# Optimization experiments

Measured on AMD Instinct MI355X. Metric: run time of the kernel, lower is better.

The kernel has to match this reference:

```python
import jax, jax.numpy as jnp
import numpy as np

N = 100000
E = 3200000
EPS = 1e-5


def setup_inputs() -> dict:
    key = jax.random.key(0)
    ks = jax.random.split(key, 12)
    inp = {
        "x": jax.random.normal(ks[0], (N, 512), dtype=jnp.float32),
        "rows": jax.random.randint(ks[1], (E,), 0, N, dtype=jnp.int32),
        "cols": jax.random.randint(ks[2], (E,), 0, N, dtype=jnp.int32),
        "adj_vals": jax.random.uniform(ks[3], (E,), dtype=jnp.float32),
        "w0": jax.random.normal(ks[4], (512, 256), dtype=jnp.float32) * (1.0 / np.sqrt(512)),
        "b0": jnp.zeros((256,), dtype=jnp.float32),
        "w1": jax.random.normal(ks[5], (256, 128), dtype=jnp.float32) * (1.0 / np.sqrt(256)),
        "b1": jnp.zeros((128,), dtype=jnp.float32),
        "dw0": jax.random.normal(ks[6], (128, 256), dtype=jnp.float32) * (1.0 / np.sqrt(128)),
        "db0": jnp.zeros((256,), dtype=jnp.float32),
        "dw1": jax.random.normal(ks[7], (256, 512), dtype=jnp.float32) * (1.0 / np.sqrt(256)),
        "db1": jnp.zeros((512,), dtype=jnp.float32),
    }
    return inp


def _spmm(rows, cols, vals, h):
    # sparse adj (COO) @ dense h : gather neighbor rows, scale, scatter-add
    return jax.ops.segment_sum(vals[:, None] * h[cols], rows, num_segments=N)


def _bn(h):
    # BatchNorm1d(affine=False, track_running_stats=False): batch stats, biased var
    m = h.mean(axis=0)
    v = h.var(axis=0)
    return (h - m) / jnp.sqrt(v + EPS)


def reference(x, rows, cols, adj_vals, w0, b0, w1, b1, dw0, db0, dw1, db1):
    # encoder: 512 -> 256 (relu, bn) -> 128
    h = _spmm(rows, cols, adj_vals, x @ w0) + b0
    h = _bn(jax.nn.relu(h))
    x_out = _spmm(rows, cols, adj_vals, h @ w1) + b1
    # decoder: relu -> 128 -> 256 (relu, bn) -> 512
    r = jax.nn.relu(x_out)
    r = _spmm(rows, cols, adj_vals, r @ dw0) + db0
    r = _bn(jax.nn.relu(r))
    x_rec = _spmm(rows, cols, adj_vals, r @ dw1) + db1
    return (x_out, x_rec)
```

## Files before the change

kernel.cpp:

```cpp
#include <hip/hip_runtime.h>


typedef _Float16 half2v __attribute__((ext_vector_type(2)));
typedef _Float16 half4v __attribute__((ext_vector_type(4)));
typedef _Float16 half8v __attribute__((ext_vector_type(8)));
typedef float f32x4 __attribute__((ext_vector_type(4)));

__global__ void cast_f32_to_f16(const float* __restrict__ in, _Float16* __restrict__ out,
                                size_t n4) {
    const size_t i = (size_t)blockIdx.x * blockDim.x + threadIdx.x;
    if (i >= n4) return;
    const float4 v = ((const float4*)in)[i];
    half4v h;
    h.x = (_Float16)v.x; h.y = (_Float16)v.y; h.z = (_Float16)v.z; h.w = (_Float16)v.w;
    ((half4v*)out)[i] = h;
}

__global__ void cast_transpose_w(const float* __restrict__ W, _Float16* __restrict__ Wt,
                                 int Kin, int Kout) {
    const int idx = blockIdx.x * blockDim.x + threadIdx.x;
    if (idx >= Kin * Kout) return;
    const int c = idx / Kin;
    const int k = idx - c * Kin;
    Wt[idx] = (_Float16)W[(size_t)k * Kout + c];
}

template <bool OUT_F16, bool HAS_BIAS>
__global__ __launch_bounds__(256) void gemm_f16(const _Float16* __restrict__ A,
                                                const _Float16* __restrict__ Wt,
                                                const float* __restrict__ bias,
                                                void* __restrict__ C,
                                                int Nrows, int Kin, int Kout) {
    __shared__ __align__(16) _Float16 As[128][40];
    __shared__ __align__(16) _Float16 Bs[128][40];
    const int tid = threadIdx.x;
    const int r0 = blockIdx.y * 128;
    const int c0 = blockIdx.x * 128;
    const int w = tid >> 6;
    const int lane = tid & 63;
    const int wm = (w >> 1) << 6;
    const int wn = (w & 1) << 6;
    const int lrow = lane & 15;
    const int lk = (lane >> 4) << 3;

    f32x4 acc[4][4];
#pragma unroll
    for (int i = 0; i < 4; ++i)
#pragma unroll
        for (int j = 0; j < 4; ++j) acc[i][j] = f32x4{0.f, 0.f, 0.f, 0.f};

    for (int k0 = 0; k0 < Kin; k0 += 32) {
#pragma unroll
        for (int q = 0; q < 2; ++q) {
            const int c = tid + (q << 8);
            const int row = c >> 2;
            const int kc = (c & 3) << 3;
            half8v av = half8v{0, 0, 0, 0, 0, 0, 0, 0};
            const int gr = r0 + row;
            if (gr < Nrows) av = *(const half8v*)(A + (size_t)gr * Kin + (k0 + kc));
            *(half8v*)&As[row][kc] = av;
            const half8v wv = *(const half8v*)(Wt + (size_t)(c0 + row) * Kin + (k0 + kc));
            *(half8v*)&Bs[row][kc] = wv;
        }
        __syncthreads();

        half8v af[4], bf[4];
#pragma unroll
        for (int i = 0; i < 4; ++i) af[i] = *(const half8v*)&As[wm + (i << 4) + lrow][lk];
#pragma unroll
        for (int j = 0; j < 4; ++j) bf[j] = *(const half8v*)&Bs[wn + (j << 4) + lrow][lk];
#pragma unroll
        for (int i = 0; i < 4; ++i)
#pragma unroll
            for (int j = 0; j < 4; ++j)
                acc[i][j] = __builtin_amdgcn_mfma_f32_16x16x32_f16(af[i], bf[j], acc[i][j], 0, 0, 0);
        __syncthreads();
    }

    const int crow0 = r0 + wm + ((lane >> 4) << 2);
    const int ccol0 = c0 + wn + lrow;
#pragma unroll
    for (int j = 0; j < 4; ++j) {
        const int col = ccol0 + (j << 4);
        const float bv = HAS_BIAS ? bias[col] : 0.f;
#pragma unroll
        for (int i = 0; i < 4; ++i) {
            const int rbase = crow0 + (i << 4);
#pragma unroll
            for (int qq = 0; qq < 4; ++qq) {
                const int grow = rbase + qq;
                if (grow < Nrows) {
                    const float val = acc[i][j][qq] + bv;
                    if (OUT_F16)
                        ((_Float16*)C)[(size_t)grow * Kout + col] = (_Float16)val;
                    else
                        ((float*)C)[(size_t)grow * Kout + col] = val;
                }
            }
        }
    }
}

template <bool RELU_A>
__global__ __launch_bounds__(256) void gemm_tile(const float* __restrict__ A,
                                                 const float* __restrict__ W,
                                                 const float* __restrict__ bias,
                                                 float* __restrict__ C,
                                                 int Nrows, int M, int K) {
    __shared__ float Asm[16][68];
    __shared__ float Wsm[16][68];
    const int tid = threadIdx.x;
    const int tx = tid & 15;
    const int ty = tid >> 4;
    const int row0 = blockIdx.y * 64;
    const int col0 = blockIdx.x * 64;

    float acc[4][4];
#pragma unroll
    for (int i = 0; i < 4; ++i)
#pragma unroll
        for (int j = 0; j < 4; ++j) acc[i][j] = 0.f;

    const int ar = tid >> 2;
    const int ak = (tid & 3) << 2;
    const int wr = tid >> 4;
    const int wc = (tid & 15) << 2;

    for (int k0 = 0; k0 < M; k0 += 16) {
        float4 av = make_float4(0.f, 0.f, 0.f, 0.f);
        const int grow = row0 + ar;
        if (grow < Nrows) av = *(const float4*)(A + (size_t)grow * M + (k0 + ak));
        if (RELU_A) {
            av.x = fmaxf(av.x, 0.f); av.y = fmaxf(av.y, 0.f);
            av.z = fmaxf(av.z, 0.f); av.w = fmaxf(av.w, 0.f);
        }
        Asm[ak + 0][ar] = av.x; Asm[ak + 1][ar] = av.y;
        Asm[ak + 2][ar] = av.z; Asm[ak + 3][ar] = av.w;
        float4 wv = *(const float4*)(W + (size_t)(k0 + wr) * K + (col0 + wc));
        *(float4*)&Wsm[wr][wc] = wv;
        __syncthreads();
#pragma unroll
        for (int kk = 0; kk < 16; ++kk) {
            const float4 a = *(const float4*)&Asm[kk][ty << 2];
            const float4 b = *(const float4*)&Wsm[kk][tx << 2];
            acc[0][0] += a.x * b.x; acc[0][1] += a.x * b.y; acc[0][2] += a.x * b.z; acc[0][3] += a.x * b.w;
            acc[1][0] += a.y * b.x; acc[1][1] += a.y * b.y; acc[1][2] += a.y * b.z; acc[1][3] += a.y * b.w;
            acc[2][0] += a.z * b.x; acc[2][1] += a.z * b.y; acc[2][2] += a.z * b.z; acc[2][3] += a.z * b.w;
            acc[3][0] += a.w * b.x; acc[3][1] += a.w * b.y; acc[3][2] += a.w * b.z; acc[3][3] += a.w * b.w;
        }
        __syncthreads();
    }

    float4 bv = make_float4(0.f, 0.f, 0.f, 0.f);
    if (bias != nullptr) bv = *(const float4*)(bias + col0 + (tx << 2));
#pragma unroll
    for (int i = 0; i < 4; ++i) {
        const int grow = row0 + (ty << 2) + i;
        if (grow < Nrows) {
            float4 o = make_float4(acc[i][0] + bv.x, acc[i][1] + bv.y,
                                   acc[i][2] + bv.z, acc[i][3] + bv.w);
            *(float4*)(C + (size_t)grow * K + col0 + (tx << 2)) = o;
        }
    }
}

__global__ void zero_ints(int* __restrict__ p, int n) {
    const int i = blockIdx.x * blockDim.x + threadIdx.x;
    if (i < n) p[i] = 0;
}

__global__ void hist_rows(const int* __restrict__ rows, int* __restrict__ cnt, int E) {
    const int e = blockIdx.x * blockDim.x + threadIdx.x;
    if (e < E) atomicAdd(&cnt[rows[e]], 1);
}

__global__ __launch_bounds__(256) void scan_reduce(const int* __restrict__ cnt,
                                                   int* __restrict__ blockSums, int Nrows) {
    __shared__ int sh[256];
    const int t = threadIdx.x;
    const int idx0 = blockIdx.x * 1024 + t * 4;
    int s = 0;
#pragma unroll
    for (int k = 0; k < 4; ++k) s += (idx0 + k < Nrows) ? cnt[idx0 + k] : 0;
    sh[t] = s;
    __syncthreads();
    for (int d = 128; d > 0; d >>= 1) {
        if (t < d) sh[t] += sh[t + d];
        __syncthreads();
    }
    if (t == 0) blockSums[blockIdx.x] = sh[0];
}

__global__ __launch_bounds__(256) void scan_blocksums(int* __restrict__ blockSums, int NB,
                                                      int* __restrict__ row_start, int Nrows,
                                                      int E) {
    __shared__ int sh[256];
    const int t = threadIdx.x;
    const int v = (t < NB) ? blockSums[t] : 0;
    sh[t] = v;
    __syncthreads();
    for (int d = 1; d < 256; d <<= 1) {
        int add = (t >= d) ? sh[t - d] : 0;
        __syncthreads();
        sh[t] += add;
        __syncthreads();
    }
    if (t < NB) blockSums[t] = sh[t] - v;
    if (t == 0) row_start[Nrows] = E;
}

__global__ __launch_bounds__(256) void scan_final(const int* __restrict__ cnt,
                                                  const int* __restrict__ blockSums,
                                                  int* __restrict__ row_start,
                                                  int* __restrict__ cursor, int Nrows) {
    __shared__ int sh[256];
    const int t = threadIdx.x;
    const int idx0 = blockIdx.x * 1024 + t * 4;
    int c[4];
    int mySum = 0;
#pragma unroll
    for (int k = 0; k < 4; ++k) {
        c[k] = (idx0 + k < Nrows) ? cnt[idx0 + k] : 0;
        mySum += c[k];
    }
    sh[t] = mySum;
    __syncthreads();
    for (int d = 1; d < 256; d <<= 1) {
        int add = (t >= d) ? sh[t - d] : 0;
        __syncthreads();
        sh[t] += add;
        __syncthreads();
    }
    int running = blockSums[blockIdx.x] + sh[t] - mySum;
#pragma unroll
    for (int k = 0; k < 4; ++k) {
        if (idx0 + k < Nrows) {
            row_start[idx0 + k] = running;
            cursor[idx0 + k] = running;
        }
        running += c[k];
    }
}

__global__ void scatter_edges(const int* __restrict__ rows, const int* __restrict__ cols,
                              const float* __restrict__ vals, int* __restrict__ cursor,
                              int* __restrict__ sc, float* __restrict__ sv, int E) {
    const int e = blockIdx.x * blockDim.x + threadIdx.x;
    if (e >= E) return;
    const int pos = atomicAdd(&cursor[rows[e]], 1);
    sc[pos] = cols[e];
    sv[pos] = vals[e];
}

template <int VW, bool RELU_H, bool HAS_BIAS, bool IN_H, bool OUT_H>
__global__ __launch_bounds__(256) void spmm_csr(const int* __restrict__ row_start,
                                                const int* __restrict__ sc,
                                                const float* __restrict__ sv,
                                                const void* __restrict__ Hv,
                                                const float* __restrict__ bias,
                                                void* __restrict__ outv, int Nrows, int F) {
    const int lane = threadIdx.x & 63;
    const int r = blockIdx.x * 4 + (threadIdx.x >> 6);
    if (r >= Nrows) return;
    const int s = row_start[r];
    const int e_end = row_start[r + 1];

    float acc[VW];
#pragma unroll
    for (int i = 0; i < VW; ++i) acc[i] = HAS_BIAS ? bias[lane * VW + i] : 0.f;

    const float* Hf = (const float*)Hv;
    const _Float16* Hh = (const _Float16*)Hv;

    for (int base = s; base < e_end; base += 64) {
        const int n = min(64, e_end - base);
        int cL = 0;
        float vL = 0.f;
        if (lane < n) { cL = sc[base + lane]; vL = sv[base + lane]; }
        for (int j = 0; j < n; ++j) {
            const int cj = __shfl(cL, j);
            const float vj = __shfl(vL, j);
            float h[VW];
            if (IN_H) {
                const _Float16* hp = Hh + (size_t)cj * F + lane * VW;
                if (VW == 2) {
                    const half2v hv = *(const half2v*)hp;
                    h[0] = (float)hv.x; h[1] = (float)hv.y;
                } else {
#pragma unroll
                    for (int q = 0; q < VW; q += 4) {
                        const half4v hv = *(const half4v*)(hp + q);
                        h[q + 0] = (float)hv.x; h[q + 1] = (float)hv.y;
                        h[q + 2] = (float)hv.z; h[q + 3] = (float)hv.w;
                    }
                }
            } else {
                const float* hp = Hf + (size_t)cj * F + lane * VW;
                if (VW == 2) {
                    const float2 hv = *(const float2*)hp;
                    h[0] = hv.x; h[1] = hv.y;
                } else {
#pragma unroll
                    for (int q = 0; q < VW; q += 4) {
                        const float4 hv = *(const float4*)(hp + q);
                        h[q + 0] = hv.x; h[q + 1] = hv.y; h[q + 2] = hv.z; h[q + 3] = hv.w;
                    }
                }
            }
#pragma unroll
            for (int q = 0; q < VW; ++q) {
                float hq = h[q];
                if (RELU_H) hq = fmaxf(hq, 0.f);
                acc[q] += vj * hq;
            }
        }
    }

    if (OUT_H) {
        _Float16* op = (_Float16*)outv + (size_t)r * F + lane * VW;
        if (VW == 2) {
            half2v o; o.x = (_Float16)acc[0]; o.y = (_Float16)acc[1];
            *(half2v*)op = o;
        } else {
#pragma unroll
            for (int q = 0; q < VW; q += 4) {
                half4v o;
                o.x = (_Float16)acc[q + 0]; o.y = (_Float16)acc[q + 1];
                o.z = (_Float16)acc[q + 2]; o.w = (_Float16)acc[q + 3];
                *(half4v*)(op + q) = o;
            }
        }
    } else {
        float* op = (float*)outv + (size_t)r * F + lane * VW;
        if (VW == 2) {
            *(float2*)op = make_float2(acc[0], acc[1]);
        } else {
#pragma unroll
            for (int q = 0; q < VW; q += 4)
                *(float4*)(op + q) = make_float4(acc[q], acc[q + 1], acc[q + 2], acc[q + 3]);
        }
    }
}

__global__ void fill_bias(float* __restrict__ out, const float* __restrict__ bias,
                          size_t n4, unsigned maskF4) {
    const size_t i = (size_t)blockIdx.x * blockDim.x + threadIdx.x;
    if (i >= n4) return;
    const int cb = (int)(i & maskF4) << 2;
    ((float4*)out)[i] = *(const float4*)(bias + cb);
}

__global__ void zero_floats4(float* __restrict__ out, size_t n4) {
    const size_t i = (size_t)blockIdx.x * blockDim.x + threadIdx.x;
    if (i >= n4) return;
    ((float4*)out)[i] = make_float4(0.f, 0.f, 0.f, 0.f);
}

template <bool RELU_H>
__global__ void spmm_edges(const int* __restrict__ rows, const int* __restrict__ cols,
                           const float* __restrict__ vals, const float* __restrict__ H,
                           float* __restrict__ out, int E, int F, int log2chunks) {
    const size_t idx = (size_t)blockIdx.x * blockDim.x + threadIdx.x;
    const int e = (int)(idx >> log2chunks);
    if (e >= E) return;
    const int c = (int)(idx & ((1u << log2chunks) - 1u));
    const int dst = rows[e];
    const int src = cols[e];
    const float v = vals[e];
    float4 h = *(const float4*)(H + (size_t)src * F + (c << 2));
    if (RELU_H) {
        h.x = fmaxf(h.x, 0.f); h.y = fmaxf(h.y, 0.f);
        h.z = fmaxf(h.z, 0.f); h.w = fmaxf(h.w, 0.f);
    }
    float* o = out + (size_t)dst * F + (c << 2);
    atomicAdd(o + 0, v * h.x);
    atomicAdd(o + 1, v * h.y);
    atomicAdd(o + 2, v * h.z);
    atomicAdd(o + 3, v * h.w);
}

__global__ void zero_stats(float* __restrict__ p) { p[threadIdx.x] = 0.f; }

__global__ void bn_stats(const float* __restrict__ H, float* __restrict__ stats, int Nrows) {
    const int c = threadIdx.x;
    float s = 0.f, q = 0.f;
    for (int n = blockIdx.x; n < Nrows; n += gridDim.x) {
        float h = H[(size_t)n * 256 + c];
        h = fmaxf(h, 0.f);
        s += h;
        q += h * h;
    }
    atomicAdd(&stats[c], s);
    atomicAdd(&stats[256 + c], q);
}

__global__ void bn_finalize(float* __restrict__ stats, float invN) {
    const int c = threadIdx.x;
    const float m = stats[c] * invN;
    const float q = stats[256 + c] * invN;
    const float var = q - m * m;
    stats[512 + c] = m;
    stats[768 + c] = rsqrtf(var + 1e-5f);
}

template <bool OUT_H>
__global__ void bn_apply(const float* __restrict__ H, const float* __restrict__ stats,
                         void* __restrict__ outv, size_t n4) {
    const size_t i = (size_t)blockIdx.x * blockDim.x + threadIdx.x;
    if (i >= n4) return;
    const int cb = (int)(i & 63u) << 2;
    const float4 h = ((const float4*)H)[i];
    const float4 m = *(const float4*)(stats + 512 + cb);
    const float4 s = *(const float4*)(stats + 768 + cb);
    float4 o;
    o.x = (fmaxf(h.x, 0.f) - m.x) * s.x;
    o.y = (fmaxf(h.y, 0.f) - m.y) * s.y;
    o.z = (fmaxf(h.z, 0.f) - m.z) * s.z;
    o.w = (fmaxf(h.w, 0.f) - m.w) * s.w;
    if (OUT_H) {
        half4v oh;
        oh.x = (_Float16)o.x; oh.y = (_Float16)o.y;
        oh.z = (_Float16)o.z; oh.w = (_Float16)o.w;
        ((half4v*)outv)[i] = oh;
    } else {
        ((float4*)outv)[i] = o;
    }
}

extern "C" void kernel_launch(void* const* d_in, const int* in_sizes, int n_in,
                              void* d_out, int out_size, void* d_ws, size_t ws_size,
                              hipStream_t stream) {
    const float* x    = (const float*)d_in[0];
    const int*   rows = (const int*)d_in[1];
    const int*   cols = (const int*)d_in[2];
    const float* vals = (const float*)d_in[3];
    const float* w0   = (const float*)d_in[4];
    const float* b0   = (const float*)d_in[5];
    const float* w1   = (const float*)d_in[6];
    const float* b1   = (const float*)d_in[7];
    const float* dw0  = (const float*)d_in[8];
    const float* db0  = (const float*)d_in[9];
    const float* dw1  = (const float*)d_in[10];
    const float* db1  = (const float*)d_in[11];

    const int N = in_sizes[0] / 512;
    const int E = in_sizes[1];

    float* xout  = (float*)d_out;
    float* rec   = xout + (size_t)N * 128;
    float* recA  = rec;
    float* recB  = rec + (size_t)N * 256;
    float* wsbig = (float*)d_ws;
    float* stats = wsbig + (size_t)N * 512;

    int*   row_start = (int*)(stats + 1024);
    int*   cursor    = row_start + (N + 1);
    int*   blockSums = cursor + N;
    int*   sc        = blockSums + 256;
    float* sv        = (float*)(sc + E);

    _Float16* arena = (_Float16*)wsbig;
    _Float16* xh   = arena;
    _Float16* t0h  = arena + (size_t)N * 512;
    _Float16* t2h  = arena;
    _Float16* t3h  = arena + (size_t)N * 256;
    _Float16* sh   = arena + (size_t)N * 384;
    _Float16* r3h  = arena;
    _Float16* uh   = arena + (size_t)N * 256;
    _Float16* w0t  = arena + (size_t)N * 768;
    _Float16* w1t  = w0t + 512 * 256;
    _Float16* dw0t = w1t + 256 * 128;
    _Float16* dw1t = dw0t + 128 * 256;

    const size_t needed =
        ((size_t)N * 512 + 1024 + (size_t)(N + 1) + (size_t)N + 256 + 2 * (size_t)E) * 4;
    const bool use_csr = ws_size >= needed;

    const dim3 blk(256);
    const int NB = (N + 1023) / 1024;
    const int egrid = (E + 255) / 256;
    const int rowgrid = (N + 3) / 4;
    const int gyM = (N + 127) / 128;

    if (use_csr) {
        zero_ints<<<dim3((N + 255) / 256), blk, 0, stream>>>(cursor, N);
        hist_rows<<<dim3(egrid), blk, 0, stream>>>(rows, cursor, E);
        scan_reduce<<<dim3(NB), blk, 0, stream>>>(cursor, blockSums, N);
        scan_blocksums<<<dim3(1), blk, 0, stream>>>(blockSums, NB, row_start, N, E);
        scan_final<<<dim3(NB), blk, 0, stream>>>(cursor, blockSums, row_start, cursor, N);
        scatter_edges<<<dim3(egrid), blk, 0, stream>>>(rows, cols, vals, cursor, sc, sv, E);

        {
            const size_t n4 = (size_t)N * 512 / 4;
            cast_f32_to_f16<<<dim3((unsigned)((n4 + 255) / 256)), blk, 0, stream>>>(x, xh, n4);
        }
        cast_transpose_w<<<dim3((512 * 256 + 255) / 256), blk, 0, stream>>>(w0, w0t, 512, 256);
        cast_transpose_w<<<dim3((256 * 128 + 255) / 256), blk, 0, stream>>>(w1, w1t, 256, 128);
        cast_transpose_w<<<dim3((128 * 256 + 255) / 256), blk, 0, stream>>>(dw0, dw0t, 128, 256);
        cast_transpose_w<<<dim3((256 * 512 + 255) / 256), blk, 0, stream>>>(dw1, dw1t, 256, 512);

        gemm_f16<true, false><<<dim3(2, gyM), blk, 0, stream>>>(xh, w0t, nullptr, t0h, N, 512, 256);
        spmm_csr<4, false, true, true, false><<<dim3(rowgrid), blk, 0, stream>>>(
            row_start, sc, sv, t0h, b0, recA, N, 256);
        zero_stats<<<dim3(1), dim3(512), 0, stream>>>(stats);
        bn_stats<<<dim3(512), blk, 0, stream>>>(recA, stats, N);
        bn_finalize<<<dim3(1), blk, 0, stream>>>(stats, 1.0f / (float)N);
        bn_apply<true><<<dim3((unsigned)(((size_t)N * 64 + 255) / 256)), blk, 0, stream>>>(
            recA, stats, t2h, (size_t)N * 64);
        gemm_f16<true, false><<<dim3(1, gyM), blk, 0, stream>>>(t2h, w1t, nullptr, t3h, N, 256, 128);
        spmm_csr<2, false, true, true, false><<<dim3(rowgrid), blk, 0, stream>>>(
            row_start, sc, sv, t3h, b1, xout, N, 128);
        spmm_csr<2, true, false, false, true><<<dim3(rowgrid), blk, 0, stream>>>(
            row_start, sc, sv, xout, nullptr, sh, N, 128);
        gemm_f16<false, true><<<dim3(2, gyM), blk, 0, stream>>>(sh, dw0t, db0, recB, N, 128, 256);
        zero_stats<<<dim3(1), dim3(512), 0, stream>>>(stats);
        bn_stats<<<dim3(512), blk, 0, stream>>>(recB, stats, N);
        bn_finalize<<<dim3(1), blk, 0, stream>>>(stats, 1.0f / (float)N);
        bn_apply<true><<<dim3((unsigned)(((size_t)N * 64 + 255) / 256)), blk, 0, stream>>>(
            recB, stats, r3h, (size_t)N * 64);
        spmm_csr<4, false, false, true, true><<<dim3(rowgrid), blk, 0, stream>>>(
            row_start, sc, sv, r3h, nullptr, uh, N, 256);
        gemm_f16<false, true><<<dim3(4, gyM), blk, 0, stream>>>(uh, dw1t, db1, rec, N, 256, 512);
        return;
    }

    const int gy = (N + 63) / 64;
    gemm_tile<false><<<dim3(256 / 64, gy), blk, 0, stream>>>(x, w0, nullptr, recA, N, 512, 256);
    {
        const size_t n4 = (size_t)N * 256 / 4;
        fill_bias<<<dim3((unsigned)((n4 + 255) / 256)), blk, 0, stream>>>(recB, b0, n4, 63u);
        const size_t tot = (size_t)E * 64;
        spmm_edges<false><<<dim3((unsigned)((tot + 255) / 256)), blk, 0, stream>>>(
            rows, cols, vals, recA, recB, E, 256, 6);
    }
    zero_stats<<<dim3(1), dim3(512), 0, stream>>>(stats);
    bn_stats<<<dim3(512), blk, 0, stream>>>(recB, stats, N);
    bn_finalize<<<dim3(1), blk, 0, stream>>>(stats, 1.0f / (float)N);
    bn_apply<false><<<dim3((unsigned)(((size_t)N * 64 + 255) / 256)), blk, 0, stream>>>(
        recB, stats, recA, (size_t)N * 64);
    gemm_tile<false><<<dim3(128 / 64, gy), blk, 0, stream>>>(recA, w1, nullptr, wsbig, N, 256, 128);
    {
        const size_t n4 = (size_t)N * 128 / 4;
        fill_bias<<<dim3((unsigned)((n4 + 255) / 256)), blk, 0, stream>>>(xout, b1, n4, 31u);
        const size_t tot = (size_t)E * 32;
        spmm_edges<false><<<dim3((unsigned)((tot + 255) / 256)), blk, 0, stream>>>(
            rows, cols, vals, wsbig, xout, E, 128, 5);
    }
    {
        const size_t n4 = (size_t)N * 128 / 4;
        zero_floats4<<<dim3((unsigned)((n4 + 255) / 256)), blk, 0, stream>>>(wsbig, n4);
        const size_t tot = (size_t)E * 32;
        spmm_edges<true><<<dim3((unsigned)((tot + 255) / 256)), blk, 0, stream>>>(
            rows, cols, vals, xout, wsbig, E, 128, 5);
    }
    gemm_tile<false><<<dim3(256 / 64, gy), blk, 0, stream>>>(wsbig, dw0, db0, recA, N, 128, 256);
    zero_stats<<<dim3(1), dim3(512), 0, stream>>>(stats);
    bn_stats<<<dim3(512), blk, 0, stream>>>(recA, stats, N);
    bn_finalize<<<dim3(1), blk, 0, stream>>>(stats, 1.0f / (float)N);
    bn_apply<false><<<dim3((unsigned)(((size_t)N * 64 + 255) / 256)), blk, 0, stream>>>(
        recA, stats, recB, (size_t)N * 64);
    {
        const size_t n4 = (size_t)N * 256 / 4;
        zero_floats4<<<dim3((unsigned)((n4 + 255) / 256)), blk, 0, stream>>>(wsbig, n4);
        const size_t tot = (size_t)E * 64;
        spmm_edges<false><<<dim3((unsigned)((tot + 255) / 256)), blk, 0, stream>>>(
            rows, cols, vals, recB, wsbig, E, 256, 6);
    }
    gemm_tile<false><<<dim3(512 / 64, gy), blk, 0, stream>>>(wsbig, dw1, db1, rec, N, 256, 512);
}
```

Before: 2.052 ms.

## Fuse x cast into GEMM, interleave CSR edges, mirror relu fp16 output, vectorize BN stats

The first GEMM now loads fp32 x directly and converts it to fp16 while staging tiles, which removes the standalone cast kernel and its N×512 fp16 round trip. CSR column indices and values are packed into one int2 array, so each edge needs a single 8-byte load. The x_out SpMM also writes a relu'd fp16 copy, letting the next SpMM gather half-width rows instead of fp32. bn_stats switches to float4 loads with a shared-memory reduction across four row slices, at the cost of an extra mirror write and slightly different fp16 rounding placement.

```diff
diff --git a/kernel.cpp b/kernel.cpp
--- a/kernel.cpp
+++ b/kernel.cpp
@@ -5,16 +5,6 @@
 typedef _Float16 half4v __attribute__((ext_vector_type(4)));
 typedef _Float16 half8v __attribute__((ext_vector_type(8)));
 typedef float f32x4 __attribute__((ext_vector_type(4)));
-
-__global__ void cast_f32_to_f16(const float* __restrict__ in, _Float16* __restrict__ out,
-                                size_t n4) {
-    const size_t i = (size_t)blockIdx.x * blockDim.x + threadIdx.x;
-    if (i >= n4) return;
-    const float4 v = ((const float4*)in)[i];
-    half4v h;
-    h.x = (_Float16)v.x; h.y = (_Float16)v.y; h.z = (_Float16)v.z; h.w = (_Float16)v.w;
-    ((half4v*)out)[i] = h;
-}
 
 __global__ void cast_transpose_w(const float* __restrict__ W, _Float16* __restrict__ Wt,
                                  int Kin, int Kout) {
@@ -25,8 +15,8 @@
     Wt[idx] = (_Float16)W[(size_t)k * Kout + c];
 }
 
-template <bool OUT_F16, bool HAS_BIAS>
-__global__ __launch_bounds__(256) void gemm_f16(const _Float16* __restrict__ A,
+template <bool A_F32, bool OUT_F16, bool HAS_BIAS>
+__global__ __launch_bounds__(256) void gemm_f16(const void* __restrict__ Av,
                                                 const _Float16* __restrict__ Wt,
                                                 const float* __restrict__ bias,
                                                 void* __restrict__ C,
@@ -43,6 +33,9 @@
     const int lrow = lane & 15;
     const int lk = (lane >> 4) << 3;
 
+    const _Float16* A16 = (const _Float16*)Av;
+    const float* A32 = (const float*)Av;
+
     f32x4 acc[4][4];
 #pragma unroll
     for (int i = 0; i < 4; ++i)
@@ -55,9 +48,23 @@
             const int c = tid + (q << 8);
             const int row = c >> 2;
             const int kc = (c & 3) << 3;
-            half8v av = half8v{0, 0, 0, 0, 0, 0, 0, 0};
             const int gr = r0 + row;
-            if (gr < Nrows) av = *(const half8v*)(A + (size_t)gr * Kin + (k0 + kc));
+            half8v av;
+            if (A_F32) {
+                float4 a0 = make_float4(0.f, 0.f, 0.f, 0.f);
+                float4 a1 = make_float4(0.f, 0.f, 0.f, 0.f);
+                if (gr < Nrows) {
+                    a0 = *(const float4*)(A32 + (size_t)gr * Kin + (k0 + kc));
+                    a1 = *(const float4*)(A32 + (size_t)gr * Kin + (k0 + kc) + 4);
+                }
+                av[0] = (_Float16)a0.x; av[1] = (_Float16)a0.y;
+                av[2] = (_Float16)a0.z; av[3] = (_Float16)a0.w;
+                av[4] = (_Float16)a1.x; av[5] = (_Float16)a1.y;
+                av[6] = (_Float16)a1.z; av[7] = (_Float16)a1.w;
+            } else {
+                av = half8v{0, 0, 0, 0, 0, 0, 0, 0};
+                if (gr < Nrows) av = *(const half8v*)(A16 + (size_t)gr * Kin + (k0 + kc));
+            }
             *(half8v*)&As[row][kc] = av;
             const half8v wv = *(const half8v*)(Wt + (size_t)(c0 + row) * Kin + (k0 + kc));
             *(half8v*)&Bs[row][kc] = wv;
@@ -244,21 +251,21 @@
 
 __global__ void scatter_edges(const int* __restrict__ rows, const int* __restrict__ cols,
                               const float* __restrict__ vals, int* __restrict__ cursor,
-                              int* __restrict__ sc, float* __restrict__ sv, int E) {
+                              int2* __restrict__ svc, int E) {
     const int e = blockIdx.x * blockDim.x + threadIdx.x;
     if (e >= E) return;
     const int pos = atomicAdd(&cursor[rows[e]], 1);
-    sc[pos] = cols[e];
-    sv[pos] = vals[e];
-}
-
-template <int VW, bool RELU_H, bool HAS_BIAS, bool IN_H, bool OUT_H>
+    svc[pos] = make_int2(cols[e], __float_as_int(vals[e]));
+}
+
+template <int VW, bool RELU_H, bool HAS_BIAS, bool IN_H, bool OUT_H, bool MIRROR>
 __global__ __launch_bounds__(256) void spmm_csr(const int* __restrict__ row_start,
-                                                const int* __restrict__ sc,
-                                                const float* __restrict__ sv,
+                                                const int2* __restrict__ svc,
                                                 const void* __restrict__ Hv,
                                                 const float* __restrict__ bias,
-                                                void* __restrict__ outv, int Nrows, int F) {
+                                                void* __restrict__ outv,
+                                                _Float16* __restrict__ mir,
+                                                int Nrows, int F) {
     const int lane = threadIdx.x & 63;
     const int r = blockIdx.x * 4 + (threadIdx.x >> 6);
     if (r >= Nrows) return;
@@ -276,7 +283,11 @@
         const int n = min(64, e_end - base);
         int cL = 0;
         float vL = 0.f;
-        if (lane < n) { cL = sc[base + lane]; vL = sv[base + lane]; }
+        if (lane < n) {
+            const int2 p = svc[base + lane];
+            cL = p.x;
+            vL = __int_as_float(p.y);
+        }
         for (int j = 0; j < n; ++j) {
             const int cj = __shfl(cL, j);
             const float vj = __shfl(vL, j);
@@ -338,6 +349,25 @@
 #pragma unroll
             for (int q = 0; q < VW; q += 4)
                 *(float4*)(op + q) = make_float4(acc[q], acc[q + 1], acc[q + 2], acc[q + 3]);
+        }
+    }
+    if (MIRROR) {
+        _Float16* mp = mir + (size_t)r * F + lane * VW;
+        if (VW == 2) {
+            half2v m;
+            m.x = (_Float16)fmaxf(acc[0], 0.f);
+            m.y = (_Float16)fmaxf(acc[1], 0.f);
+            *(half2v*)mp = m;
+        } else {
+#pragma unroll
+            for (int q = 0; q < VW; q += 4) {
+                half4v m;
+                m.x = (_Float16)fmaxf(acc[q + 0], 0.f);
+                m.y = (_Float16)fmaxf(acc[q + 1], 0.f);
+                m.z = (_Float16)fmaxf(acc[q + 2], 0.f);
+                m.w = (_Float16)fmaxf(acc[q + 3], 0.f);
+                *(half4v*)(mp + q) = m;
+            }
         }
     }
 }
@@ -381,17 +411,41 @@
 
 __global__ void zero_stats(float* __restrict__ p) { p[threadIdx.x] = 0.f; }
 
-__global__ void bn_stats(const float* __restrict__ H, float* __restrict__ stats, int Nrows) {
-    const int c = threadIdx.x;
-    float s = 0.f, q = 0.f;
-    for (int n = blockIdx.x; n < Nrows; n += gridDim.x) {
-        float h = H[(size_t)n * 256 + c];
-        h = fmaxf(h, 0.f);
-        s += h;
-        q += h * h;
-    }
-    atomicAdd(&stats[c], s);
-    atomicAdd(&stats[256 + c], q);
+__global__ __launch_bounds__(256) void bn_stats(const float* __restrict__ H,
+                                                float* __restrict__ stats, int Nrows) {
+    __shared__ float shs[4][64][4];
+    __shared__ float shq[4][64][4];
+    const int t = threadIdx.x;
+    const int cg = t & 63;
+    const int rs = t >> 6;
+    float4 s = make_float4(0.f, 0.f, 0.f, 0.f);
+    float4 q = make_float4(0.f, 0.f, 0.f, 0.f);
+    for (int n = blockIdx.x * 4 + rs; n < Nrows; n += gridDim.x * 4) {
+        float4 h = *(const float4*)(H + (size_t)n * 256 + (cg << 2));
+        h.x = fmaxf(h.x, 0.f); h.y = fmaxf(h.y, 0.f);
+        h.z = fmaxf(h.z, 0.f); h.w = fmaxf(h.w, 0.f);
+        s.x += h.x; s.y += h.y; s.z += h.z; s.w += h.w;
+        q.x += h.x * h.x; q.y += h.y * h.y; q.z += h.z * h.z; q.w += h.w * h.w;
+    }
+    *(float4*)shs[rs][cg] = s;
+    *(float4*)shq[rs][cg] = q;
+    __syncthreads();
+    if (rs == 0) {
+        float4 S = make_float4(0.f, 0.f, 0.f, 0.f);
+        float4 Q = make_float4(0.f, 0.f, 0.f, 0.f);
+#pragma unroll
+        for (int k = 0; k < 4; ++k) {
+            const float4 a = *(const float4*)shs[k][cg];
+            const float4 b = *(const float4*)shq[k][cg];
+            S.x += a.x; S.y += a.y; S.z += a.z; S.w += a.w;
+            Q.x += b.x; Q.y += b.y; Q.z += b.z; Q.w += b.w;
+        }
+        const int c0 = cg << 2;
+        atomicAdd(&stats[c0 + 0], S.x); atomicAdd(&stats[c0 + 1], S.y);
+        atomicAdd(&stats[c0 + 2], S.z); atomicAdd(&stats[c0 + 3], S.w);
+        atomicAdd(&stats[256 + c0 + 0], Q.x); atomicAdd(&stats[256 + c0 + 1], Q.y);
+        atomicAdd(&stats[256 + c0 + 2], Q.z); atomicAdd(&stats[256 + c0 + 3], Q.w);
+    }
 }
 
 __global__ void bn_finalize(float* __restrict__ stats, float invN) {
@@ -456,14 +510,13 @@
     int*   row_start = (int*)(stats + 1024);
     int*   cursor    = row_start + (N + 1);
     int*   blockSums = cursor + N;
-    int*   sc        = blockSums + 256;
-    float* sv        = (float*)(sc + E);
+    int2*  svc = (int2*)(((uintptr_t)(blockSums + 256) + 15u) & ~(uintptr_t)15u);
 
     _Float16* arena = (_Float16*)wsbig;
-    _Float16* xh   = arena;
     _Float16* t0h  = arena + (size_t)N * 512;
     _Float16* t2h  = arena;
     _Float16* t3h  = arena + (size_t)N * 256;
+    _Float16* xoh  = arena;
     _Float16* sh   = arena + (size_t)N * 384;
     _Float16* r3h  = arena;
     _Float16* uh   = arena + (size_t)N * 256;
@@ -473,7 +526,8 @@
     _Float16* dw1t = dw0t + 128 * 256;
 
     const size_t needed =
-        ((size_t)N * 512 + 1024 + (size_t)(N + 1) + (size_t)N + 256 + 2 * (size_t)E) * 4;
+        ((size_t)N * 512 + 1024 + (size_t)(N + 1) + (size_t)N + 256) * 4 + 16 +
+        (size_t)E * 8;
     const bool use_csr = ws_size >= needed;
 
     const dim3 blk(256);
@@ -488,39 +542,39 @@
         scan_reduce<<<dim3(NB), blk, 0, stream>>>(cursor, blockSums, N);
         scan_blocksums<<<dim3(1), blk, 0, stream>>>(blockSums, NB, row_start, N, E);
         scan_final<<<dim3(NB), blk, 0, stream>>>(cursor, blockSums, row_start, cursor, N);
-        scatter_edges<<<dim3(egrid), blk, 0, stream>>>(rows, cols, vals, cursor, sc, sv, E);
-
-        {
-            const size_t n4 = (size_t)N * 512 / 4;
-            cast_f32_to_f16<<<dim3((unsigned)((n4 + 255) / 256)), blk, 0, stream>>>(x, xh, n4);
-        }
+        scatter_edges<<<dim3(egrid), blk, 0, stream>>>(rows, cols, vals, cursor, svc, E);
+
         cast_transpose_w<<<dim3((512 * 256 + 255) / 256), blk, 0, stream>>>(w0, w0t, 512, 256);
         cast_transpose_w<<<dim3((256 * 128 + 255) / 256), blk, 0, stream>>>(w1, w1t, 256, 128);
         cast_transpose_w<<<dim3((128 * 256 + 255) / 256), blk, 0, stream>>>(dw0, dw0t, 128, 256);
         cast_transpose_w<<<dim3((256 * 512 + 255) / 256), blk, 0, stream>>>(dw1, dw1t, 256, 512);
 
-        gemm_f16<true, false><<<dim3(2, gyM), blk, 0, stream>>>(xh, w0t, nullptr, t0h, N, 512, 256);
-        spmm_csr<4, false, true, true, false><<<dim3(rowgrid), blk, 0, stream>>>(
-            row_start, sc, sv, t0h, b0, recA, N, 256);
+        gemm_f16<true, true, false><<<dim3(2, gyM), blk, 0, stream>>>(
+            x, w0t, nullptr, t0h, N, 512, 256);
+        spmm_csr<4, false, true, true, false, false><<<dim3(rowgrid), blk, 0, stream>>>(
+            row_start, svc, t0h, b0, recA, nullptr, N, 256);
         zero_stats<<<dim3(1), dim3(512), 0, stream>>>(stats);
         bn_stats<<<dim3(512), blk, 0, stream>>>(recA, stats, N);
         bn_finalize<<<dim3(1), blk, 0, stream>>>(stats, 1.0f / (float)N);
         bn_apply<true><<<dim3((unsigned)(((size_t)N * 64 + 255) / 256)), blk, 0, stream>>>(
             recA, stats, t2h, (size_t)N * 64);
-        gemm_f16<true, false><<<dim3(1, gyM), blk, 0, stream>>>(t2h, w1t, nullptr, t3h, N, 256, 128);
-        spmm_csr<2, false, true, true, false><<<dim3(rowgrid), blk, 0, stream>>>(
-            row_start, sc, sv, t3h, b1, xout, N, 128);
-        spmm_csr<2, true, false, false, true><<<dim3(rowgrid), blk, 0, stream>>>(
-            row_start, sc, sv, xout, nullptr, sh, N, 128);
-        gemm_f16<false, true><<<dim3(2, gyM), blk, 0, stream>>>(sh, dw0t, db0, recB, N, 128, 256);
+        gemm_f16<false, true, false><<<dim3(1, gyM), blk, 0, stream>>>(
+            t2h, w1t, nullptr, t3h, N, 256, 128);
+        spmm_csr<2, false, true, true, false, true><<<dim3(rowgrid), blk, 0, stream>>>(
+            row_start, svc, t3h, b1, xout, xoh, N, 128);
+        spmm_csr<2, false, false, true, true, false><<<dim3(rowgrid), blk, 0, stream>>>(
+            row_start, svc, xoh, nullptr, sh, nullptr, N, 128);
+        gemm_f16<false, false, true><<<dim3(2, gyM), blk, 0, stream>>>(
+            sh, dw0t, db0, recB, N, 128, 256);
         zero_stats<<<dim3(1), dim3(512), 0, stream>>>(stats);
         bn_stats<<<dim3(512), blk, 0, stream>>>(recB, stats, N);
         bn_finalize<<<dim3(1), blk, 0, stream>>>(stats, 1.0f / (float)N);
         bn_apply<true><<<dim3((unsigned)(((size_t)N * 64 + 255) / 256)), blk, 0, stream>>>(
             recB, stats, r3h, (size_t)N * 64);
-        spmm_csr<4, false, false, true, true><<<dim3(rowgrid), blk, 0, stream>>>(
-            row_start, sc, sv, r3h, nullptr, uh, N, 256);
-        gemm_f16<false, true><<<dim3(4, gyM), blk, 0, stream>>>(uh, dw1t, db1, rec, N, 256, 512);
+        spmm_csr<4, false, false, true, true, false><<<dim3(rowgrid), blk, 0, stream>>>(
+            row_start, svc, r3h, nullptr, uh, nullptr, N, 256);
+        gemm_f16<false, false, true><<<dim3(4, gyM), blk, 0, stream>>>(
+            uh, dw1t, db1, rec, N, 256, 512);
         return;
     }
 
```

Result: faster. 2.006 ms (-2.2%).
